# Optimization experiments

Measured on AMD Instinct MI355X. Metric: run time of the kernel, lower is better.

## Reference

```python
import jax, jax.numpy as jnp
import numpy as np

N_NODES = 100000
N_EDGES = 3200000


def gcn_conv(x, edge_index, W, b, n_nodes):
    # PyG GCNConv default: add self-loops, symmetric degree normalization,
    # linear transform, scatter-add aggregation at target nodes, add bias.
    src = jnp.concatenate([edge_index[0], jnp.arange(n_nodes, dtype=edge_index.dtype)])
    dst = jnp.concatenate([edge_index[1], jnp.arange(n_nodes, dtype=edge_index.dtype)])
    deg = jax.ops.segment_sum(jnp.ones_like(dst, dtype=x.dtype), dst, num_segments=n_nodes)
    dinv = jnp.where(deg > 0, jax.lax.rsqrt(jnp.maximum(deg, 1e-12)), 0.0)
    norm = dinv[src] * dinv[dst]            # [E+N]
    h = x @ W                               # [N, F_out]
    msg = h[src] * norm[:, None]            # gather + scale
    out = jax.ops.segment_sum(msg, dst, num_segments=n_nodes)
    return out + b


def setup_inputs() -> dict:
    key = jax.random.key(0)
    k1, k2, k3, k4 = jax.random.split(key, 4)
    x = jax.random.normal(k1, (N_NODES, 2), dtype=jnp.float32)
    edge_index = jax.random.randint(k2, (2, N_EDGES), 0, N_NODES, dtype=jnp.int64)
    # Glorot-ish init for weights, zero bias (PyG default zeros bias).
    W1 = jax.random.normal(k3, (2, 16), dtype=jnp.float32) * (1.0 / np.sqrt(2.0))
    b1 = jnp.zeros((16,), dtype=jnp.float32)
    W2 = jax.random.normal(k4, (16, 2), dtype=jnp.float32) * (1.0 / np.sqrt(16.0))
    b2 = jnp.zeros((2,), dtype=jnp.float32)
    return {"x": x, "edge_index": edge_index, "W1": W1, "b1": b1, "W2": W2, "b2": b2}


def reference(x, edge_index, W1, b1, W2, b2):
    n = x.shape[0]
    h = gcn_conv(x, edge_index, W1, b1, n)
    h = jax.nn.relu(h)
    h = gcn_conv(h, edge_index, W2, b2, n)
    return jax.nn.log_softmax(h, axis=1)
```

## Files before the change

### kernel.cpp

```cpp
#include <hip/hip_runtime.h>
#include <math.h>


#define BLK 256
#define NTILE 512
#define EPTMAX 6400
#define MAXB 512


__global__ void k_hist(const int* __restrict__ dst, int* __restrict__ table,
                       int e, int ept, int nbkt) {
    __shared__ int h[MAXB];
    int tile = blockIdx.x;
    for (int i = threadIdx.x; i < MAXB; i += BLK) h[i] = 0;
    __syncthreads();
    int lo = tile * ept;
    int hi = min(lo + ept, e);
    for (int i = lo + 4 * threadIdx.x; i < hi; i += 4 * BLK) {
        int4 d4 = *(const int4*)(dst + i);
        atomicAdd(&h[d4.x >> 8], 1);
        atomicAdd(&h[d4.y >> 8], 1);
        atomicAdd(&h[d4.z >> 8], 1);
        atomicAdd(&h[d4.w >> 8], 1);
    }
    __syncthreads();
    for (int i = threadIdx.x; i < nbkt; i += BLK)
        table[tile * nbkt + i] = h[i];
}

__global__ void k_scan_col(int* __restrict__ table, int* __restrict__ tot, int nbkt) {
    __shared__ int wsum[NTILE / 64];
    int b = blockIdx.x;
    int t = threadIdx.x;
    int v = table[t * nbkt + b];
    int x = v;
    int lane = t & 63;
#pragma unroll
    for (int ofs = 1; ofs < 64; ofs <<= 1) {
        int y = __shfl_up(x, ofs, 64);
        if (lane >= ofs) x += y;
    }
    if (lane == 63) wsum[t >> 6] = x;
    __syncthreads();
    if (t < NTILE / 64) {
        int s = wsum[t];
        int w = s;
#pragma unroll
        for (int ofs = 1; ofs < NTILE / 64; ofs <<= 1) {
            int y = __shfl_up(w, ofs, 64);
            if (t >= ofs) w += y;
        }
        wsum[t] = w - s;
    }
    __syncthreads();
    int incl = x + wsum[t >> 6];
    table[t * nbkt + b] = incl - v;
    if (t == NTILE - 1) tot[b] = incl;
}

__global__ void k_scan_tot(const int* __restrict__ tot, int* __restrict__ bkt_off, int nbkt) {
    __shared__ int wsum[MAXB / 64];
    int t = threadIdx.x;
    int v = (t < nbkt) ? tot[t] : 0;
    int x = v;
    int lane = t & 63;
#pragma unroll
    for (int ofs = 1; ofs < 64; ofs <<= 1) {
        int y = __shfl_up(x, ofs, 64);
        if (lane >= ofs) x += y;
    }
    if (lane == 63) wsum[t >> 6] = x;
    __syncthreads();
    if (t < MAXB / 64) {
        int s = wsum[t];
        int w = s;
#pragma unroll
        for (int ofs = 1; ofs < MAXB / 64; ofs <<= 1) {
            int y = __shfl_up(w, ofs, 64);
            if (t >= ofs) w += y;
        }
        wsum[t] = w - s;
    }
    __syncthreads();
    int incl = x + wsum[t >> 6];
    if (t < nbkt) bkt_off[t] = incl - v;
    if (t == nbkt - 1) bkt_off[nbkt] = incl;
}

__global__ void k_scatter(const int* __restrict__ src, const int* __restrict__ dst,
                          const int* __restrict__ table, const int* __restrict__ tot,
                          const int* __restrict__ bkt_off, unsigned* __restrict__ sorted,
                          int e, int ept, int nbkt) {
    __shared__ int cur[MAXB];
    __shared__ int base2[MAXB];
    __shared__ unsigned stage[EPTMAX];
    __shared__ unsigned short stage_b[EPTMAX];
    __shared__ int wpart[BLK / 64];
    int tile = blockIdx.x;
    int t = threadIdx.x;
    int lo = tile * ept;
    int hi = min(lo + ept, e);
    int total = hi - lo;

    int b0 = 2 * t, b1 = 2 * t + 1;
    int c0 = 0, c1 = 0, g0 = 0, g1 = 0;
    if (b0 < nbkt) {
        int base = table[tile * nbkt + b0];
        int next = (tile < NTILE - 1) ? table[(tile + 1) * nbkt + b0] : tot[b0];
        c0 = next - base;
        g0 = bkt_off[b0] + base;
    }
    if (b1 < nbkt) {
        int base = table[tile * nbkt + b1];
        int next = (tile < NTILE - 1) ? table[(tile + 1) * nbkt + b1] : tot[b1];
        c1 = next - base;
        g1 = bkt_off[b1] + base;
    }
    int p = c0 + c1;
    int x = p;
    int lane = t & 63;
#pragma unroll
    for (int ofs = 1; ofs < 64; ofs <<= 1) {
        int y = __shfl_up(x, ofs, 64);
        if (lane >= ofs) x += y;
    }
    if (lane == 63) wpart[t >> 6] = x;
    __syncthreads();
    if (t < BLK / 64) {
        int s = wpart[t];
        int w = s;
#pragma unroll
        for (int ofs = 1; ofs < BLK / 64; ofs <<= 1) {
            int y = __shfl_up(w, ofs, 64);
            if (t >= ofs) w += y;
        }
        wpart[t] = w - s;
    }
    __syncthreads();
    int E = x + wpart[t >> 6] - p;
    cur[b0] = E;
    cur[b1] = E + c0;
    if (b0 < nbkt) base2[b0] = g0 - E;
    if (b1 < nbkt) base2[b1] = g1 - (E + c0);
    __syncthreads();

    for (int i = lo + 4 * t; i < hi; i += 4 * BLK) {
        int4 s4 = *(const int4*)(src + i);
        int4 d4 = *(const int4*)(dst + i);
        int b, pos;
        b = d4.x >> 8; pos = atomicAdd(&cur[b], 1);
        stage[pos] = (unsigned)s4.x | ((unsigned)(d4.x & 255) << 17); stage_b[pos] = (unsigned short)b;
        b = d4.y >> 8; pos = atomicAdd(&cur[b], 1);
        stage[pos] = (unsigned)s4.y | ((unsigned)(d4.y & 255) << 17); stage_b[pos] = (unsigned short)b;
        b = d4.z >> 8; pos = atomicAdd(&cur[b], 1);
        stage[pos] = (unsigned)s4.z | ((unsigned)(d4.z & 255) << 17); stage_b[pos] = (unsigned short)b;
        b = d4.w >> 8; pos = atomicAdd(&cur[b], 1);
        stage[pos] = (unsigned)s4.w | ((unsigned)(d4.w & 255) << 17); stage_b[pos] = (unsigned short)b;
    }
    __syncthreads();
    for (int j = t; j < total; j += BLK) {
        int b = stage_b[j];
        sorted[base2[b] + j] = stage[j];
    }
}

__global__ __launch_bounds__(1024) void k_bsort(
        const unsigned* __restrict__ sorted, const int* __restrict__ bkt_off,
        const float* __restrict__ x, float* __restrict__ dinv,
        float* __restrict__ xp, unsigned* __restrict__ nsorted,
        int* __restrict__ nodeoff, int n) {
    __shared__ int cnt[256];
    __shared__ int cur[256];
    __shared__ int wsum[16];
    int b = blockIdx.x, t = threadIdx.x;
    if (t < 256) cnt[t] = 0;
    __syncthreads();
    int lo = bkt_off[b], hi = bkt_off[b + 1];
    int la = lo & ~3;
    for (int i = la + 4 * t; i < hi; i += 4 * 1024) {
        uint4 r = *(const uint4*)(sorted + i);
        if (i >= lo && i + 4 <= hi) {
            atomicAdd(&cnt[r.x >> 17], 1);
            atomicAdd(&cnt[r.y >> 17], 1);
            atomicAdd(&cnt[r.z >> 17], 1);
            atomicAdd(&cnt[r.w >> 17], 1);
        } else {
            if (i + 0 >= lo && i + 0 < hi) atomicAdd(&cnt[r.x >> 17], 1);
            if (i + 1 >= lo && i + 1 < hi) atomicAdd(&cnt[r.y >> 17], 1);
            if (i + 2 >= lo && i + 2 < hi) atomicAdd(&cnt[r.z >> 17], 1);
            if (i + 3 >= lo && i + 3 < hi) atomicAdd(&cnt[r.w >> 17], 1);
        }
    }
    __syncthreads();
    int c = (t < 256) ? cnt[t] : 0;
    int node = (b << 8) + t;
    if (t < 256 && node < n) {
        float d = rsqrtf((float)c + 1.0f);
        dinv[node] = d;
        float2 xv = ((const float2*)x)[node];
        ((float2*)xp)[node] = make_float2(d * xv.x, d * xv.y);
    }
    int xsc = c;
    int lane = t & 63;
#pragma unroll
    for (int ofs = 1; ofs < 64; ofs <<= 1) {
        int y = __shfl_up(xsc, ofs, 64);
        if (lane >= ofs) xsc += y;
    }
    if (lane == 63) wsum[t >> 6] = xsc;
    __syncthreads();
    if (t < 4) {
        int s = wsum[t];
        int w = s;
#pragma unroll
        for (int ofs = 1; ofs < 4; ofs <<= 1) {
            int y = __shfl_up(w, ofs, 64);
            if (t >= ofs) w += y;
        }
        wsum[t] = w - s;
    }
    __syncthreads();
    if (t < 256) {
        int excl = xsc + wsum[t >> 6] - c;
        cur[t] = excl;
        nodeoff[(b << 8) + t] = lo + excl;
    }
    __syncthreads();
    for (int i = la + 4 * t; i < hi; i += 4 * 1024) {
        uint4 r = *(const uint4*)(sorted + i);
        if (i >= lo && i + 4 <= hi) {
            int p0 = atomicAdd(&cur[r.x >> 17], 1); nsorted[lo + p0] = r.x & 0x1FFFFu;
            int p1 = atomicAdd(&cur[r.y >> 17], 1); nsorted[lo + p1] = r.y & 0x1FFFFu;
            int p2 = atomicAdd(&cur[r.z >> 17], 1); nsorted[lo + p2] = r.z & 0x1FFFFu;
            int p3 = atomicAdd(&cur[r.w >> 17], 1); nsorted[lo + p3] = r.w & 0x1FFFFu;
        } else {
            if (i + 0 >= lo && i + 0 < hi) { int p0 = atomicAdd(&cur[r.x >> 17], 1); nsorted[lo + p0] = r.x & 0x1FFFFu; }
            if (i + 1 >= lo && i + 1 < hi) { int p1 = atomicAdd(&cur[r.y >> 17], 1); nsorted[lo + p1] = r.y & 0x1FFFFu; }
            if (i + 2 >= lo && i + 2 < hi) { int p2 = atomicAdd(&cur[r.z >> 17], 1); nsorted[lo + p2] = r.z & 0x1FFFFu; }
            if (i + 3 >= lo && i + 3 < hi) { int p3 = atomicAdd(&cur[r.w >> 17], 1); nsorted[lo + p3] = r.w & 0x1FFFFu; }
        }
    }
}


__global__ void k_agg1(const unsigned* __restrict__ nsorted, const int* __restrict__ nodeoff,
                       const float* __restrict__ xp, const float* __restrict__ dinv,
                       const float* __restrict__ W1, const float* __restrict__ b1,
                       const float* __restrict__ W2, float* __restrict__ gp, int n) {
    int t = threadIdx.x;
    int nd = (blockIdx.x << 8) + (blockIdx.y << 6) + (t >> 2);
    int q = t & 3;
    if (nd >= n) return;
    int start = nodeoff[nd], end = nodeoff[nd + 1];
    const float2* xp2 = (const float2*)xp;
    float sx = 0.f, sy = 0.f;
    for (int p = (start & ~3) + 4 * q; p < end; p += 16) {
        uint4 r = *(const uint4*)(nsorted + p);
        if (p >= start && p + 4 <= end) {
            float2 f0 = xp2[r.x], f1 = xp2[r.y], f2 = xp2[r.z], f3 = xp2[r.w];
            sx += (f0.x + f1.x) + (f2.x + f3.x);
            sy += (f0.y + f1.y) + (f2.y + f3.y);
        } else {
            if (p + 0 >= start && p + 0 < end) { float2 f = xp2[r.x]; sx += f.x; sy += f.y; }
            if (p + 1 >= start && p + 1 < end) { float2 f = xp2[r.y]; sx += f.x; sy += f.y; }
            if (p + 2 >= start && p + 2 < end) { float2 f = xp2[r.z]; sx += f.x; sy += f.y; }
            if (p + 3 >= start && p + 3 < end) { float2 f = xp2[r.w]; sx += f.x; sy += f.y; }
        }
    }
    sx += __shfl_xor(sx, 1); sy += __shfl_xor(sy, 1);
    sx += __shfl_xor(sx, 2); sy += __shfl_xor(sy, 2);
    if (q == 0) {
        float d = dinv[nd];
        float2 xv = xp2[nd];
        float ax = d * (sx + xv.x), ay = d * (sy + xv.y);
        float g0 = 0.f, g1 = 0.f;
#pragma unroll
        for (int f = 0; f < 16; ++f) {
            float h = fmaf(ax, W1[f], fmaf(ay, W1[16 + f], b1[f]));
            h = fmaxf(h, 0.0f);
            g0 = fmaf(h, W2[2 * f + 0], g0);
            g1 = fmaf(h, W2[2 * f + 1], g1);
        }
        ((float2*)gp)[nd] = make_float2(d * g0, d * g1);
    }
}

__global__ void k_agg2(const unsigned* __restrict__ nsorted, const int* __restrict__ nodeoff,
                       const float* __restrict__ gp, const float* __restrict__ dinv,
                       const float* __restrict__ b2, float* __restrict__ out, int n) {
    int t = threadIdx.x;
    int nd = (blockIdx.x << 8) + (blockIdx.y << 6) + (t >> 2);
    int q = t & 3;
    if (nd >= n) return;
    int start = nodeoff[nd], end = nodeoff[nd + 1];
    const float2* gp2 = (const float2*)gp;
    float sx = 0.f, sy = 0.f;
    for (int p = (start & ~3) + 4 * q; p < end; p += 16) {
        uint4 r = *(const uint4*)(nsorted + p);
        if (p >= start && p + 4 <= end) {
            float2 f0 = gp2[r.x], f1 = gp2[r.y], f2 = gp2[r.z], f3 = gp2[r.w];
            sx += (f0.x + f1.x) + (f2.x + f3.x);
            sy += (f0.y + f1.y) + (f2.y + f3.y);
        } else {
            if (p + 0 >= start && p + 0 < end) { float2 f = gp2[r.x]; sx += f.x; sy += f.y; }
            if (p + 1 >= start && p + 1 < end) { float2 f = gp2[r.y]; sx += f.x; sy += f.y; }
            if (p + 2 >= start && p + 2 < end) { float2 f = gp2[r.z]; sx += f.x; sy += f.y; }
            if (p + 3 >= start && p + 3 < end) { float2 f = gp2[r.w]; sx += f.x; sy += f.y; }
        }
    }
    sx += __shfl_xor(sx, 1); sy += __shfl_xor(sy, 1);
    sx += __shfl_xor(sx, 2); sy += __shfl_xor(sy, 2);
    if (q == 0) {
        float d = dinv[nd];
        float2 gv = gp2[nd];
        float z0 = d * (sx + gv.x) + b2[0];
        float z1 = d * (sy + gv.y) + b2[1];
        float m = fmaxf(z0, z1);
        float lse = m + logf(expf(z0 - m) + expf(z1 - m));
        ((float2*)out)[nd] = make_float2(z0 - lse, z1 - lse);
    }
}

extern "C" void kernel_launch(void* const* d_in, const int* in_sizes, int n_in,
                              void* d_out, int out_size, void* d_ws, size_t ws_size,
                              hipStream_t stream) {
    const float* x  = (const float*)d_in[0];
    const int*   ei = (const int*)d_in[1];
    const float* W1 = (const float*)d_in[2];
    const float* b1 = (const float*)d_in[3];
    const float* W2 = (const float*)d_in[4];
    const float* b2 = (const float*)d_in[5];
    float* out = (float*)d_out;

    const int n = in_sizes[0] / 2;
    const int e = in_sizes[1] / 2;
    const int* src = ei;
    const int* dst = ei + e;

    const int nbkt = (n + 255) >> 8;
    int ept = (((e + NTILE - 1) / NTILE) + 3) & ~3;

    char* base = (char*)d_ws;
    size_t off = 0;
    auto take = [&](size_t bytes) { char* p = base + off; off += (bytes + 255) & ~(size_t)255; return p; };
    unsigned* sorted  = (unsigned*)take(((size_t)e + 8) * 4);
    int*      table   = (int*)take((size_t)NTILE * nbkt * 4);
    int*      tot     = (int*)take((size_t)MAXB * 4);
    int*      bkt_off = (int*)take((size_t)(MAXB + 1) * 4);
    unsigned* nsorted = (unsigned*)take(((size_t)e + 8) * 4);
    int*      nodeoff = (int*)take((size_t)(nbkt * 256 + 64) * 4);
    float*    dinv    = (float*)take((size_t)n * 4);
    float*    xp      = (float*)take((size_t)n * 8);
    float*    gp      = (float*)take((size_t)n * 8);

    dim3 gagg(nbkt, 4);

    k_hist    <<<NTILE, BLK, 0, stream>>>(dst, table, e, ept, nbkt);
    k_scan_col<<<nbkt, NTILE, 0, stream>>>(table, tot, nbkt);
    k_scan_tot<<<1, MAXB, 0, stream>>>(tot, bkt_off, nbkt);
    k_scatter <<<NTILE, BLK, 0, stream>>>(src, dst, table, tot, bkt_off, sorted, e, ept, nbkt);
    k_bsort   <<<nbkt, 1024, 0, stream>>>(sorted, bkt_off, x, dinv, xp, nsorted, nodeoff, n);
    k_agg1    <<<gagg, BLK, 0, stream>>>(nsorted, nodeoff, xp, dinv, W1, b1, W2, gp, n);
    k_agg2    <<<gagg, BLK, 0, stream>>>(nsorted, nodeoff, gp, dinv, b2, out, n);
}
```

Before: 157.1 us.

## Drop per-node sort; aggregate per bucket with shared-memory float atomics

Removes the second-level per-node counting sort (k_bsort) and its nsorted/nodeoff buffers. Aggregation kernels now run one 1024-thread block per 256-node bucket and accumulate messages into shared-memory float atomics keyed by the node's low 8 bits. Degrees are computed with global atomics inside the histogram pass, and dinv/xp are produced in the column-scan kernel, with a memset added. This trades a full sort pass over the edges for 3.2M global integer atomics and many LDS float atomics with contention, and the floating-point summation order becomes nondeterministic.

```diff
diff --git a/kernel.cpp b/kernel.cpp
--- a/kernel.cpp
+++ b/kernel.cpp
@@ -9,7 +9,7 @@
 
 
 __global__ void k_hist(const int* __restrict__ dst, int* __restrict__ table,
-                       int e, int ept, int nbkt) {
+                       int* __restrict__ deg, int e, int ept, int nbkt) {
     __shared__ int h[MAXB];
     int tile = blockIdx.x;
     for (int i = threadIdx.x; i < MAXB; i += BLK) h[i] = 0;
@@ -22,25 +22,32 @@
         atomicAdd(&h[d4.y >> 8], 1);
         atomicAdd(&h[d4.z >> 8], 1);
         atomicAdd(&h[d4.w >> 8], 1);
+        atomicAdd(&deg[d4.x], 1);
+        atomicAdd(&deg[d4.y], 1);
+        atomicAdd(&deg[d4.z], 1);
+        atomicAdd(&deg[d4.w], 1);
     }
     __syncthreads();
     for (int i = threadIdx.x; i < nbkt; i += BLK)
         table[tile * nbkt + i] = h[i];
 }
 
-__global__ void k_scan_col(int* __restrict__ table, int* __restrict__ tot, int nbkt) {
+__global__ void k_scan_col(int* __restrict__ table, int* __restrict__ tot,
+                           const int* __restrict__ deg, const float* __restrict__ x,
+                           float* __restrict__ dinv, float* __restrict__ xp,
+                           int nbkt, int n) {
     __shared__ int wsum[NTILE / 64];
     int b = blockIdx.x;
     int t = threadIdx.x;
     int v = table[t * nbkt + b];
-    int x = v;
+    int x0 = v;
     int lane = t & 63;
 #pragma unroll
     for (int ofs = 1; ofs < 64; ofs <<= 1) {
-        int y = __shfl_up(x, ofs, 64);
-        if (lane >= ofs) x += y;
-    }
-    if (lane == 63) wsum[t >> 6] = x;
+        int y = __shfl_up(x0, ofs, 64);
+        if (lane >= ofs) x0 += y;
+    }
+    if (lane == 63) wsum[t >> 6] = x0;
     __syncthreads();
     if (t < NTILE / 64) {
         int s = wsum[t];
@@ -53,9 +60,17 @@
         wsum[t] = w - s;
     }
     __syncthreads();
-    int incl = x + wsum[t >> 6];
+    int incl = x0 + wsum[t >> 6];
     table[t * nbkt + b] = incl - v;
     if (t == NTILE - 1) tot[b] = incl;
+
+    int id = b * NTILE + t;
+    if (id < n) {
+        float d = rsqrtf((float)deg[id] + 1.0f);
+        dinv[id] = d;
+        float2 xv = ((const float2*)x)[id];
+        ((float2*)xp)[id] = make_float2(d * xv.x, d * xv.y);
+    }
 }
 
 __global__ void k_scan_tot(const int* __restrict__ tot, int* __restrict__ bkt_off, int nbkt) {
@@ -164,115 +179,44 @@
     }
 }
 
-__global__ __launch_bounds__(1024) void k_bsort(
+
+__global__ __launch_bounds__(1024) void k_agg1(
         const unsigned* __restrict__ sorted, const int* __restrict__ bkt_off,
-        const float* __restrict__ x, float* __restrict__ dinv,
-        float* __restrict__ xp, unsigned* __restrict__ nsorted,
-        int* __restrict__ nodeoff, int n) {
-    __shared__ int cnt[256];
-    __shared__ int cur[256];
-    __shared__ int wsum[16];
+        const float* __restrict__ xp, const float* __restrict__ dinv,
+        const float* __restrict__ W1, const float* __restrict__ b1,
+        const float* __restrict__ W2, float* __restrict__ gp, int n) {
+    __shared__ float accx[256];
+    __shared__ float accy[256];
     int b = blockIdx.x, t = threadIdx.x;
-    if (t < 256) cnt[t] = 0;
+    if (t < 256) { accx[t] = 0.f; accy[t] = 0.f; }
     __syncthreads();
     int lo = bkt_off[b], hi = bkt_off[b + 1];
     int la = lo & ~3;
+    const float2* xp2 = (const float2*)xp;
     for (int i = la + 4 * t; i < hi; i += 4 * 1024) {
         uint4 r = *(const uint4*)(sorted + i);
         if (i >= lo && i + 4 <= hi) {
-            atomicAdd(&cnt[r.x >> 17], 1);
-            atomicAdd(&cnt[r.y >> 17], 1);
-            atomicAdd(&cnt[r.z >> 17], 1);
-            atomicAdd(&cnt[r.w >> 17], 1);
+            float2 f0 = xp2[r.x & 0x1FFFFu];
+            float2 f1 = xp2[r.y & 0x1FFFFu];
+            float2 f2 = xp2[r.z & 0x1FFFFu];
+            float2 f3 = xp2[r.w & 0x1FFFFu];
+            atomicAdd(&accx[r.x >> 17], f0.x); atomicAdd(&accy[r.x >> 17], f0.y);
+            atomicAdd(&accx[r.y >> 17], f1.x); atomicAdd(&accy[r.y >> 17], f1.y);
+            atomicAdd(&accx[r.z >> 17], f2.x); atomicAdd(&accy[r.z >> 17], f2.y);
+            atomicAdd(&accx[r.w >> 17], f3.x); atomicAdd(&accy[r.w >> 17], f3.y);
         } else {
-            if (i + 0 >= lo && i + 0 < hi) atomicAdd(&cnt[r.x >> 17], 1);
-            if (i + 1 >= lo && i + 1 < hi) atomicAdd(&cnt[r.y >> 17], 1);
-            if (i + 2 >= lo && i + 2 < hi) atomicAdd(&cnt[r.z >> 17], 1);
-            if (i + 3 >= lo && i + 3 < hi) atomicAdd(&cnt[r.w >> 17], 1);
-        }
-    }
-    __syncthreads();
-    int c = (t < 256) ? cnt[t] : 0;
-    int node = (b << 8) + t;
-    if (t < 256 && node < n) {
-        float d = rsqrtf((float)c + 1.0f);
-        dinv[node] = d;
-        float2 xv = ((const float2*)x)[node];
-        ((float2*)xp)[node] = make_float2(d * xv.x, d * xv.y);
-    }
-    int xsc = c;
-    int lane = t & 63;
-#pragma unroll
-    for (int ofs = 1; ofs < 64; ofs <<= 1) {
-        int y = __shfl_up(xsc, ofs, 64);
-        if (lane >= ofs) xsc += y;
-    }
-    if (lane == 63) wsum[t >> 6] = xsc;
-    __syncthreads();
-    if (t < 4) {
-        int s = wsum[t];
-        int w = s;
-#pragma unroll
-        for (int ofs = 1; ofs < 4; ofs <<= 1) {
-            int y = __shfl_up(w, ofs, 64);
-            if (t >= ofs) w += y;
-        }
-        wsum[t] = w - s;
-    }
-    __syncthreads();
-    if (t < 256) {
-        int excl = xsc + wsum[t >> 6] - c;
-        cur[t] = excl;
-        nodeoff[(b << 8) + t] = lo + excl;
-    }
-    __syncthreads();
-    for (int i = la + 4 * t; i < hi; i += 4 * 1024) {
-        uint4 r = *(const uint4*)(sorted + i);
-        if (i >= lo && i + 4 <= hi) {
-            int p0 = atomicAdd(&cur[r.x >> 17], 1); nsorted[lo + p0] = r.x & 0x1FFFFu;
-            int p1 = atomicAdd(&cur[r.y >> 17], 1); nsorted[lo + p1] = r.y & 0x1FFFFu;
-            int p2 = atomicAdd(&cur[r.z >> 17], 1); nsorted[lo + p2] = r.z & 0x1FFFFu;
-            int p3 = atomicAdd(&cur[r.w >> 17], 1); nsorted[lo + p3] = r.w & 0x1FFFFu;
-        } else {
-            if (i + 0 >= lo && i + 0 < hi) { int p0 = atomicAdd(&cur[r.x >> 17], 1); nsorted[lo + p0] = r.x & 0x1FFFFu; }
-            if (i + 1 >= lo && i + 1 < hi) { int p1 = atomicAdd(&cur[r.y >> 17], 1); nsorted[lo + p1] = r.y & 0x1FFFFu; }
-            if (i + 2 >= lo && i + 2 < hi) { int p2 = atomicAdd(&cur[r.z >> 17], 1); nsorted[lo + p2] = r.z & 0x1FFFFu; }
-            if (i + 3 >= lo && i + 3 < hi) { int p3 = atomicAdd(&cur[r.w >> 17], 1); nsorted[lo + p3] = r.w & 0x1FFFFu; }
-        }
-    }
-}
-
-
-__global__ void k_agg1(const unsigned* __restrict__ nsorted, const int* __restrict__ nodeoff,
-                       const float* __restrict__ xp, const float* __restrict__ dinv,
-                       const float* __restrict__ W1, const float* __restrict__ b1,
-                       const float* __restrict__ W2, float* __restrict__ gp, int n) {
-    int t = threadIdx.x;
-    int nd = (blockIdx.x << 8) + (blockIdx.y << 6) + (t >> 2);
-    int q = t & 3;
-    if (nd >= n) return;
-    int start = nodeoff[nd], end = nodeoff[nd + 1];
-    const float2* xp2 = (const float2*)xp;
-    float sx = 0.f, sy = 0.f;
-    for (int p = (start & ~3) + 4 * q; p < end; p += 16) {
-        uint4 r = *(const uint4*)(nsorted + p);
-        if (p >= start && p + 4 <= end) {
-            float2 f0 = xp2[r.x], f1 = xp2[r.y], f2 = xp2[r.z], f3 = xp2[r.w];
-            sx += (f0.x + f1.x) + (f2.x + f3.x);
-            sy += (f0.y + f1.y) + (f2.y + f3.y);
-        } else {
-            if (p + 0 >= start && p + 0 < end) { float2 f = xp2[r.x]; sx += f.x; sy += f.y; }
-            if (p + 1 >= start && p + 1 < end) { float2 f = xp2[r.y]; sx += f.x; sy += f.y; }
-            if (p + 2 >= start && p + 2 < end) { float2 f = xp2[r.z]; sx += f.x; sy += f.y; }
-            if (p + 3 >= start && p + 3 < end) { float2 f = xp2[r.w]; sx += f.x; sy += f.y; }
-        }
-    }
-    sx += __shfl_xor(sx, 1); sy += __shfl_xor(sy, 1);
-    sx += __shfl_xor(sx, 2); sy += __shfl_xor(sy, 2);
-    if (q == 0) {
+            if (i + 0 >= lo && i + 0 < hi) { float2 f = xp2[r.x & 0x1FFFFu]; atomicAdd(&accx[r.x >> 17], f.x); atomicAdd(&accy[r.x >> 17], f.y); }
+            if (i + 1 >= lo && i + 1 < hi) { float2 f = xp2[r.y & 0x1FFFFu]; atomicAdd(&accx[r.y >> 17], f.x); atomicAdd(&accy[r.y >> 17], f.y); }
+            if (i + 2 >= lo && i + 2 < hi) { float2 f = xp2[r.z & 0x1FFFFu]; atomicAdd(&accx[r.z >> 17], f.x); atomicAdd(&accy[r.z >> 17], f.y); }
+            if (i + 3 >= lo && i + 3 < hi) { float2 f = xp2[r.w & 0x1FFFFu]; atomicAdd(&accx[r.w >> 17], f.x); atomicAdd(&accy[r.w >> 17], f.y); }
+        }
+    }
+    __syncthreads();
+    int nd = (b << 8) + t;
+    if (t < 256 && nd < n) {
         float d = dinv[nd];
         float2 xv = xp2[nd];
-        float ax = d * (sx + xv.x), ay = d * (sy + xv.y);
+        float ax = d * (accx[t] + xv.x), ay = d * (accy[t] + xv.y);
         float g0 = 0.f, g1 = 0.f;
 #pragma unroll
         for (int f = 0; f < 16; ++f) {
@@ -285,36 +229,43 @@
     }
 }
 
-__global__ void k_agg2(const unsigned* __restrict__ nsorted, const int* __restrict__ nodeoff,
-                       const float* __restrict__ gp, const float* __restrict__ dinv,
-                       const float* __restrict__ b2, float* __restrict__ out, int n) {
-    int t = threadIdx.x;
-    int nd = (blockIdx.x << 8) + (blockIdx.y << 6) + (t >> 2);
-    int q = t & 3;
-    if (nd >= n) return;
-    int start = nodeoff[nd], end = nodeoff[nd + 1];
+__global__ __launch_bounds__(1024) void k_agg2(
+        const unsigned* __restrict__ sorted, const int* __restrict__ bkt_off,
+        const float* __restrict__ gp, const float* __restrict__ dinv,
+        const float* __restrict__ b2, float* __restrict__ out, int n) {
+    __shared__ float accx[256];
+    __shared__ float accy[256];
+    int b = blockIdx.x, t = threadIdx.x;
+    if (t < 256) { accx[t] = 0.f; accy[t] = 0.f; }
+    __syncthreads();
+    int lo = bkt_off[b], hi = bkt_off[b + 1];
+    int la = lo & ~3;
     const float2* gp2 = (const float2*)gp;
-    float sx = 0.f, sy = 0.f;
-    for (int p = (start & ~3) + 4 * q; p < end; p += 16) {
-        uint4 r = *(const uint4*)(nsorted + p);
-        if (p >= start && p + 4 <= end) {
-            float2 f0 = gp2[r.x], f1 = gp2[r.y], f2 = gp2[r.z], f3 = gp2[r.w];
-            sx += (f0.x + f1.x) + (f2.x + f3.x);
-            sy += (f0.y + f1.y) + (f2.y + f3.y);
+    for (int i = la + 4 * t; i < hi; i += 4 * 1024) {
+        uint4 r = *(const uint4*)(sorted + i);
+        if (i >= lo && i + 4 <= hi) {
+            float2 f0 = gp2[r.x & 0x1FFFFu];
+            float2 f1 = gp2[r.y & 0x1FFFFu];
+            float2 f2 = gp2[r.z & 0x1FFFFu];
+            float2 f3 = gp2[r.w & 0x1FFFFu];
+            atomicAdd(&accx[r.x >> 17], f0.x); atomicAdd(&accy[r.x >> 17], f0.y);
+            atomicAdd(&accx[r.y >> 17], f1.x); atomicAdd(&accy[r.y >> 17], f1.y);
+            atomicAdd(&accx[r.z >> 17], f2.x); atomicAdd(&accy[r.z >> 17], f2.y);
+            atomicAdd(&accx[r.w >> 17], f3.x); atomicAdd(&accy[r.w >> 17], f3.y);
         } else {
-            if (p + 0 >= start && p + 0 < end) { float2 f = gp2[r.x]; sx += f.x; sy += f.y; }
-            if (p + 1 >= start && p + 1 < end) { float2 f = gp2[r.y]; sx += f.x; sy += f.y; }
-            if (p + 2 >= start && p + 2 < end) { float2 f = gp2[r.z]; sx += f.x; sy += f.y; }
-            if (p + 3 >= start && p + 3 < end) { float2 f = gp2[r.w]; sx += f.x; sy += f.y; }
-        }
-    }
-    sx += __shfl_xor(sx, 1); sy += __shfl_xor(sy, 1);
-    sx += __shfl_xor(sx, 2); sy += __shfl_xor(sy, 2);
-    if (q == 0) {
+            if (i + 0 >= lo && i + 0 < hi) { float2 f = gp2[r.x & 0x1FFFFu]; atomicAdd(&accx[r.x >> 17], f.x); atomicAdd(&accy[r.x >> 17], f.y); }
+            if (i + 1 >= lo && i + 1 < hi) { float2 f = gp2[r.y & 0x1FFFFu]; atomicAdd(&accx[r.y >> 17], f.x); atomicAdd(&accy[r.y >> 17], f.y); }
+            if (i + 2 >= lo && i + 2 < hi) { float2 f = gp2[r.z & 0x1FFFFu]; atomicAdd(&accx[r.z >> 17], f.x); atomicAdd(&accy[r.z >> 17], f.y); }
+            if (i + 3 >= lo && i + 3 < hi) { float2 f = gp2[r.w & 0x1FFFFu]; atomicAdd(&accx[r.w >> 17], f.x); atomicAdd(&accy[r.w >> 17], f.y); }
+        }
+    }
+    __syncthreads();
+    int nd = (b << 8) + t;
+    if (t < 256 && nd < n) {
         float d = dinv[nd];
         float2 gv = gp2[nd];
-        float z0 = d * (sx + gv.x) + b2[0];
-        float z1 = d * (sy + gv.y) + b2[1];
+        float z0 = d * (accx[t] + gv.x) + b2[0];
+        float z1 = d * (accy[t] + gv.y) + b2[1];
         float m = fmaxf(z0, z1);
         float lse = m + logf(expf(z0 - m) + expf(z1 - m));
         ((float2*)out)[nd] = make_float2(z0 - lse, z1 - lse);
@@ -347,19 +298,16 @@
     int*      table   = (int*)take((size_t)NTILE * nbkt * 4);
     int*      tot     = (int*)take((size_t)MAXB * 4);
     int*      bkt_off = (int*)take((size_t)(MAXB + 1) * 4);
-    unsigned* nsorted = (unsigned*)take(((size_t)e + 8) * 4);
-    int*      nodeoff = (int*)take((size_t)(nbkt * 256 + 64) * 4);
+    int*      deg     = (int*)take((size_t)n * 4);
     float*    dinv    = (float*)take((size_t)n * 4);
     float*    xp      = (float*)take((size_t)n * 8);
     float*    gp      = (float*)take((size_t)n * 8);
 
-    dim3 gagg(nbkt, 4);
-
-    k_hist    <<<NTILE, BLK, 0, stream>>>(dst, table, e, ept, nbkt);
-    k_scan_col<<<nbkt, NTILE, 0, stream>>>(table, tot, nbkt);
+    hipMemsetAsync(deg, 0, (size_t)n * 4, stream);
+    k_hist    <<<NTILE, BLK, 0, stream>>>(dst, table, deg, e, ept, nbkt);
+    k_scan_col<<<nbkt, NTILE, 0, stream>>>(table, tot, deg, x, dinv, xp, nbkt, n);
     k_scan_tot<<<1, MAXB, 0, stream>>>(tot, bkt_off, nbkt);
     k_scatter <<<NTILE, BLK, 0, stream>>>(src, dst, table, tot, bkt_off, sorted, e, ept, nbkt);
-    k_bsort   <<<nbkt, 1024, 0, stream>>>(sorted, bkt_off, x, dinv, xp, nsorted, nodeoff, n);
-    k_agg1    <<<gagg, BLK, 0, stream>>>(nsorted, nodeoff, xp, dinv, W1, b1, W2, gp, n);
-    k_agg2    <<<gagg, BLK, 0, stream>>>(nsorted, nodeoff, gp, dinv, b2, out, n);
-}
+    k_agg1    <<<nbkt, 1024, 0, stream>>>(sorted, bkt_off, xp, dinv, W1, b1, W2, gp, n);
+    k_agg2    <<<nbkt, 1024, 0, stream>>>(sorted, bkt_off, gp, dinv, b2, out, n);
+}
```

Result: slower. 315.4 us (+100.7%).
